# Optimization experiments

Measured on AMD Instinct MI355X. Metric: run time of the kernel, lower is better.

Reference implementation:

```python
import jax, jax.numpy as jnp
import numpy as np

VOCAB, D_MODEL, HEADS, PAD_ID = 32000, 512, 8, 0
D_K = D_MODEL // HEADS
EPS = 1e-5


def pos_encoding(T, d):
    pos = jnp.arange(T, dtype=jnp.float32)[:, None]              # [T,1]
    freqs = 1.0 / (10000.0 ** (jnp.arange(0, d, 2, dtype=jnp.float32) / d))
    ang = pos * freqs                                            # [T,d/2]
    pe = jnp.zeros((T, d), dtype=jnp.float32)
    pe = pe.at[:, 0::2].set(jnp.sin(ang)).at[:, 1::2].set(jnp.cos(ang))
    return pe


def layer_norm(x, g, b):
    mu = jnp.mean(x, axis=-1, keepdims=True)
    var = jnp.var(x, axis=-1, keepdims=True)
    return (x - mu) * jax.lax.rsqrt(var + EPS) * g + b


def setup_inputs() -> dict:
    key = jax.random.key(0)
    ks = jax.random.split(key, 12)
    B, T = 4, 2048
    s = 0.02
    inp = {
        "tokens": jax.random.randint(ks[0], (B, T), 0, VOCAB),
        "emb": jax.random.normal(ks[1], (VOCAB, D_MODEL), jnp.float32) * s,
        "wq": jax.random.normal(ks[2], (D_MODEL, D_MODEL), jnp.float32) * s,
        "bq": jnp.zeros((D_MODEL,), jnp.float32),
        "wk": jax.random.normal(ks[3], (D_MODEL, D_MODEL), jnp.float32) * s,
        "bk": jnp.zeros((D_MODEL,), jnp.float32),
        "wv": jax.random.normal(ks[4], (D_MODEL, D_MODEL), jnp.float32) * s,
        "bv": jnp.zeros((D_MODEL,), jnp.float32),
        "wo": jax.random.normal(ks[5], (D_MODEL, D_MODEL), jnp.float32) * s,
        "bo": jnp.zeros((D_MODEL,), jnp.float32),
        "w1": jax.random.normal(ks[6], (D_MODEL, 2 * D_MODEL), jnp.float32) * s,
        "b1": jnp.zeros((2 * D_MODEL,), jnp.float32),
        "w2": jax.random.normal(ks[7], (2 * D_MODEL, D_MODEL), jnp.float32) * s,
        "b2": jnp.zeros((D_MODEL,), jnp.float32),
        "ln1_g": jnp.ones((D_MODEL,), jnp.float32),
        "ln1_b": jnp.zeros((D_MODEL,), jnp.float32),
        "ln2_g": jnp.ones((D_MODEL,), jnp.float32),
        "ln2_b": jnp.zeros((D_MODEL,), jnp.float32),
    }
    return inp


def reference(tokens, emb, wq, bq, wk, bk, wv, bv, wo, bo,
              w1, b1, w2, b2, ln1_g, ln1_b, ln2_g, ln2_b):
    B, T = tokens.shape
    x = emb[tokens] * jnp.sqrt(jnp.float32(D_MODEL))             # [B,T,D]
    x = x + pos_encoding(T, D_MODEL)[None]                       # add PE
    q = (x @ wq + bq).reshape(B, T, HEADS, D_K)
    k = (x @ wk + bk).reshape(B, T, HEADS, D_K)
    v = (x @ wv + bv).reshape(B, T, HEADS, D_K)
    scores = jnp.einsum("bqhd,bkhd->bhqk", q, k) / jnp.sqrt(jnp.float32(D_K))
    key_pad_mask = tokens == PAD_ID                              # [B,T]
    neg = jnp.finfo(scores.dtype).min
    scores = jnp.where(key_pad_mask[:, None, None, :], neg, scores)
    attn = jax.nn.softmax(scores, axis=-1)                       # [B,H,T,T]
    av = jnp.einsum("bhqk,bkhd->bqhd", attn, v).reshape(B, T, D_MODEL)
    av = av @ wo + bo
    h = layer_norm(av + x, ln1_g, ln1_b)
    ff = jax.nn.relu(h @ w1 + b1) @ w2 + b2
    out = layer_norm(h + ff, ln2_g, ln2_b)
    return out, key_pad_mask
```

## Files before the change

kernel.cpp:

```cpp
#include <hip/hip_runtime.h>
#include <hip/hip_bf16.h>
#include <math.h>

#define D_MODEL 512
#define HEADS   8
#define D_K     64
#define T_SEQ   2048
#define B_SZ    4
#define NROWS   (B_SZ * T_SEQ)
#define KVB     64

#define BM 128
#define BN 128
#define BKG 64

typedef __attribute__((ext_vector_type(8))) short short8;
typedef __attribute__((ext_vector_type(4))) float f32x4;
typedef __attribute__((ext_vector_type(4))) ushort bf16x4;
typedef __attribute__((ext_vector_type(2))) unsigned int u32x2;

typedef __attribute__((address_space(1))) const unsigned int as1_uint;
typedef __attribute__((address_space(3))) unsigned int as3_uint;

__device__ __forceinline__ ushort f2bf(float f) {
    union { float f; unsigned u; } v; v.f = f;
    unsigned u = v.u;
    unsigned r = (u + 0x7FFFu + ((u >> 16) & 1u)) >> 16;
    return (ushort)r;
}
__device__ __forceinline__ float bf2f(ushort u) {
    union { unsigned u; float f; } v; v.u = ((unsigned)u) << 16;
    return v.f;
}
__device__ __forceinline__ unsigned pk_bf16(float lo, float hi) {
    unsigned r;
    asm("v_cvt_pk_bf16_f32 %0, %1, %2" : "=v"(r) : "v"(lo), "v"(hi));
    return r;
}

__global__ __launch_bounds__(256) void k_prep(
    const int* __restrict__ tokens, const float* __restrict__ emb,
    const float* __restrict__ wq, const float* __restrict__ wk,
    const float* __restrict__ wv, const float* __restrict__ wo,
    const float* __restrict__ w1, const float* __restrict__ w2,
    const float* __restrict__ bq, const float* __restrict__ bk,
    const float* __restrict__ bv,
    float* __restrict__ xf, ushort* __restrict__ xb, float* __restrict__ mask_out,
    ushort* __restrict__ wqkvT, ushort* __restrict__ woT,
    ushort* __restrict__ w1T, ushort* __restrict__ w2T,
    float* __restrict__ bqkv, float qsc)
{
    __shared__ ushort tls[32][33];
    int bid = blockIdx.x, tid = threadIdx.x;
    if (bid < 4096) {
        int row = bid * 2 + (tid >> 7);
        int t   = row & (T_SEQ - 1);
        int tok = tokens[row];
        int t2  = tid & 127;
        if (t2 == 0) mask_out[row] = (tok == 0) ? 1.0f : 0.0f;
        const float* e = emb + (size_t)tok * D_MODEL;
#pragma unroll
        for (int i = 0; i < 4; ++i) {
            int d = t2 + 128 * i;
            float freq = exp2f(-(float)(d & ~1) * 0.025952563240330564f);
            float sn, cs;
            sincosf((float)t * freq, &sn, &cs);
            float x = e[d] * 22.627416997969522f + ((d & 1) ? cs : sn);
            xf[(size_t)row * D_MODEL + d] = x;
            xb[(size_t)row * D_MODEL + d] = f2bf(x);
        }
        return;
    }
    const float* src; ushort* dst; float scale = 1.0f; int K, N, bx, by;
    if (bid < 5120) {
        int b = bid - 4096; int z = b >> 8; int rem = b & 255;
        bx = rem & 15; by = rem >> 4; K = 512; N = 512;
        src = (z == 0) ? wq : (z == 1) ? wk : (z == 2) ? wv : wo;
        dst = (z < 3) ? wqkvT + (size_t)z * 512 * 512 : woT;
        scale = (z == 0) ? qsc : 1.0f;
    } else if (bid < 5632) {
        int b = bid - 5120; bx = b & 31; by = b >> 5; K = 512; N = 1024; src = w1; dst = w1T;
    } else if (bid < 6144) {
        int b = bid - 5632; bx = b & 15; by = b >> 4; K = 1024; N = 512; src = w2; dst = w2T;
    } else {
        int i = (bid - 6144) * 256 + tid;
        if (i < 512)       bqkv[i] = bq[i] * qsc;
        else if (i < 1024) bqkv[i] = bk[i - 512];
        else if (i < 1536) bqkv[i] = bv[i - 1024];
        return;
    }
    int tx = tid & 31, ty = tid >> 5;
    int n0 = bx * 32, k0 = by * 32;
#pragma unroll
    for (int i = 0; i < 4; ++i)
        tls[ty + i * 8][tx] = f2bf(src[(size_t)(k0 + ty + i * 8) * N + n0 + tx] * scale);
    __syncthreads();
#pragma unroll
    for (int i = 0; i < 4; ++i)
        dst[(size_t)(n0 + ty + i * 8) * K + k0 + tx] = tls[tx][ty + i * 8];
}

template<int MODE, bool RELU>
__global__ __launch_bounds__(256) void k_gemm_lds(
    const ushort* __restrict__ A, const ushort* __restrict__ BT,
    const float* __restrict__ bias, void* __restrict__ C0,
    void* __restrict__ C1, void* __restrict__ C2,
    int M, int N, int K)
{
    __shared__ __attribute__((aligned(16))) ushort As[2][BM * BKG];
    __shared__ __attribute__((aligned(16))) ushort Bs[2][BN * BKG];

    const int tid = threadIdx.x;
    const int w = tid >> 6, l = tid & 63;
    const int lr = l & 15, lg = l >> 4;
    const int wr = w >> 1, wc = w & 1;

    int bx = blockIdx.x, by = blockIdx.y;
    {
        int nx = gridDim.x, ny = gridDim.y;
        if ((ny & 7) == 0) {
            int lin = bx + nx * by;
            int xcd = lin & 7, idx = lin >> 3;
            int per = ny >> 3;
            by = xcd * per + (idx % per);
            bx = idx / per;
        }
    }
    const int brow0 = by * BM;
    const int bcol0 = bx * BN;
    const int gi0 = w * 256 + l;
    const int swz = lr & 7;

    f32x4 acc[4][4] = {};
    const int nks = K >> 6;

#define STAGE(buf, k0)                                                          \
    {                                                                           \
        _Pragma("unroll")                                                       \
        for (int i = 0; i < 4; ++i) {                                           \
            int gi = gi0 + i * 64;                                              \
            int row = gi >> 3, slot = gi & 7;                                   \
            int g = slot ^ (row & 7);                                           \
            __builtin_amdgcn_global_load_lds(                                   \
                (as1_uint*)(A + (size_t)(brow0 + row) * K + (k0) + g * 8),      \
                (as3_uint*)(&As[buf][gi * 8]), 16, 0, 0);                       \
            __builtin_amdgcn_global_load_lds(                                   \
                (as1_uint*)(BT + (size_t)(bcol0 + row) * K + (k0) + g * 8),     \
                (as3_uint*)(&Bs[buf][gi * 8]), 16, 0, 0);                       \
        }                                                                       \
    }

    STAGE(0, 0);
    __syncthreads();

    int buf = 0;
    for (int ks = 0; ks < nks; ++ks) {
        if (ks + 1 < nks) STAGE(buf ^ 1, (ks + 1) * BKG);
#pragma unroll
        for (int kk = 0; kk < 2; ++kk) {
            short8 af[4], bfr[4];
#pragma unroll
            for (int m = 0; m < 4; ++m) {
                int row = wr * 64 + m * 16 + lr;
                int slot = (kk * 4 + lg) ^ swz;
                af[m] = *(const short8*)(&As[buf][row * 64 + slot * 8]);
            }
#pragma unroll
            for (int n = 0; n < 4; ++n) {
                int row = wc * 64 + n * 16 + lr;
                int slot = (kk * 4 + lg) ^ swz;
                bfr[n] = *(const short8*)(&Bs[buf][row * 64 + slot * 8]);
            }
#pragma unroll
            for (int m = 0; m < 4; ++m)
#pragma unroll
                for (int n = 0; n < 4; ++n)
                    acc[m][n] = __builtin_amdgcn_mfma_f32_16x16x32_bf16(af[m], bfr[n], acc[m][n], 0, 0, 0);
        }
        __syncthreads();
        buf ^= 1;
    }
#undef STAGE

#pragma unroll
    for (int n = 0; n < 4; ++n) {
        int col = bcol0 + wc * 64 + n * 16 + lr;
        float bv = bias[col];
#pragma unroll
        for (int m = 0; m < 4; ++m) {
            int row0 = brow0 + wr * 64 + m * 16 + 4 * lg;
            if constexpr (MODE == 2) {
                int seg = col >> 9, lc = col & 511;
                if (seg == 2) {
                    bf16x4 pk;
#pragma unroll
                    for (int j = 0; j < 4; ++j) pk[j] = f2bf(acc[m][n][j] + bv);
                    *(bf16x4*)((ushort*)C2 + (size_t)lc * M + row0) = pk;
                } else {
                    ushort* dst = (seg == 0) ? (ushort*)C0 : (ushort*)C1;
#pragma unroll
                    for (int j = 0; j < 4; ++j)
                        dst[(size_t)(row0 + j) * 512 + lc] = f2bf(acc[m][n][j] + bv);
                }
            } else if constexpr (MODE == 0) {
#pragma unroll
                for (int j = 0; j < 4; ++j) {
                    float v = acc[m][n][j] + bv;
                    if (RELU) v = fmaxf(v, 0.0f);
                    ((ushort*)C0)[(size_t)(row0 + j) * N + col] = f2bf(v);
                }
            } else {
#pragma unroll
                for (int j = 0; j < 4; ++j)
                    ((float*)C0)[(size_t)(row0 + j) * N + col] = acc[m][n][j] + bv;
            }
        }
    }
}

__global__ __launch_bounds__(512, 4) void k_attn(
    const ushort* __restrict__ Q, const ushort* __restrict__ Kb,
    const ushort* __restrict__ Vt, const int* __restrict__ tokens,
    ushort* __restrict__ Out)
{
    __shared__ __attribute__((aligned(16))) ushort Kl[2][KVB * 64];
    __shared__ __attribute__((aligned(16))) ushort Vl[2][KVB * 64];
    __shared__ ushort Pl[8][16 * 64];
    __shared__ float  Mb[T_SEQ];
    __shared__ int    padf[T_SEQ / KVB];

    const int tid = threadIdx.x;
    const int w = tid >> 6, l = tid & 63;
    const int lr = l & 15, lg = l >> 4;
    const int swz  = lr & 7;
    const int swzP = (lr ^ (lr >> 3)) & 7;

    int lin = blockIdx.x + 16 * (blockIdx.y + 8 * blockIdx.z);
    int xcd = lin & 7, idx = lin >> 3;
    int qt = idx & 15;
    int hb = xcd * 4 + (idx >> 4);
    int h = hb & 7, b = hb >> 3;

    const int q0 = qt * 128 + w * 16;

    const int gi   = w * 64 + l;
    const int srow = gi >> 3;
    const int sg   = (gi & 7) ^ (srow & 7);
    const ushort* Ksrc = Kb + ((size_t)(b * T_SEQ) + srow) * D_MODEL + h * D_K + sg * 8;
    const ushort* Vsrc = Vt + (size_t)(h * D_K + srow) * NROWS + b * T_SEQ + sg * 8;

#define ASTAGE(bufi, kt_)                                                       \
    {                                                                           \
        __builtin_amdgcn_global_load_lds(                                       \
            (as1_uint*)(Ksrc + (size_t)(kt_) * KVB * D_MODEL),                  \
            (as3_uint*)(&Kl[bufi][gi * 8]), 16, 0, 0);                          \
        __builtin_amdgcn_global_load_lds(                                       \
            (as1_uint*)(Vsrc + (kt_) * KVB),                                    \
            (as3_uint*)(&Vl[bufi][gi * 8]), 16, 0, 0);                          \
    }

    const ushort* Qh = Q + (size_t)b * T_SEQ * D_MODEL + h * D_K;
    short8 aq[2];
#pragma unroll
    for (int c2 = 0; c2 < 2; ++c2)
        aq[c2] = *(const short8*)(Qh + (size_t)(q0 + lr) * D_MODEL + c2 * 32 + 8 * lg);

    const int* tk = tokens + b * T_SEQ;
#pragma unroll
    for (int it = 0; it < T_SEQ / 512; ++it) {
        int i = tid + it * 512;
        bool pad = (tk[i] == 0);
        Mb[i] = pad ? -1e30f : 0.0f;
        unsigned long long bal = __ballot(pad);
        if (l == 0) padf[it * 8 + w] = (bal != 0ull);
    }

    float l_run = 0.0f;
    f32x4 acc[4] = {};

    ASTAGE(0, 0);
    __syncthreads();

    int buf = 0;
    const int NT = T_SEQ / KVB;
    for (int kt = 0; kt < NT; ++kt) {
        if (kt + 1 < NT) ASTAGE(buf ^ 1, kt + 1);

        const ushort* Kt = Kl[buf];
        const ushort* Vb = Vl[buf];
        ushort* P = Pl[w];

        f32x4 s[4];
        __builtin_amdgcn_s_setprio(1);
#pragma unroll
        for (int kb = 0; kb < 4; ++kb) {
            f32x4 sf = {};
#pragma unroll
            for (int c2 = 0; c2 < 2; ++c2) {
                short8 bk = *(const short8*)((const char*)Kt
                            + (kb * 16 + lr) * 128 + (((c2 * 4 + lg) ^ swz) * 16));
                sf = __builtin_amdgcn_mfma_f32_16x16x32_bf16(bk, aq[c2], sf, 0, 0, 0);
            }
            s[kb] = sf;
        }
        __builtin_amdgcn_s_setprio(0);

        if (padf[kt]) {
            const float* mrow = Mb + kt * KVB + 4 * lg;
#pragma unroll
            for (int kb = 0; kb < 4; ++kb) {
                f32x4 mb4 = *(const f32x4*)(mrow + kb * 16);
#pragma unroll
                for (int j = 0; j < 4; ++j) s[kb][j] += mb4[j];
            }
        }

        float pv[4][4];
        float ts = 0.0f;
#pragma unroll
        for (int kb = 0; kb < 4; ++kb)
#pragma unroll
            for (int j = 0; j < 4; ++j) {
                float pe = exp2f(s[kb][j]);
                pv[kb][j] = pe;
                ts += pe;
            }
        ts += __shfl_xor(ts, 16);
        ts += __shfl_xor(ts, 32);
        l_run += ts;

#pragma unroll
        for (int kb = 0; kb < 4; ++kb) {
            u32x2 dw;
            dw[0] = pk_bf16(pv[kb][0], pv[kb][1]);
            dw[1] = pk_bf16(pv[kb][2], pv[kb][3]);
            int g = (2 * kb + (lg >> 1)) ^ swzP;
            *(u32x2*)((char*)P + lr * 128 + g * 16 + (lg & 1) * 8) = dw;
        }

        short8 pa[2];
#pragma unroll
        for (int kk = 0; kk < 2; ++kk)
            pa[kk] = *(const short8*)((const char*)P + lr * 128 + (((kk * 4 + lg) ^ swzP) * 16));

        __builtin_amdgcn_s_setprio(1);
#pragma unroll
        for (int c = 0; c < 4; ++c)
#pragma unroll
            for (int kk = 0; kk < 2; ++kk) {
                short8 bv = *(const short8*)((const char*)Vb
                            + (c * 16 + lr) * 128 + (((kk * 4 + lg) ^ swz) * 16));
                acc[c] = __builtin_amdgcn_mfma_f32_16x16x32_bf16(bv, pa[kk], acc[c], 0, 0, 0);
            }
        __builtin_amdgcn_s_setprio(0);

        __syncthreads();
        buf ^= 1;
    }
#undef ASTAGE

    float rl = 1.0f / l_run;
    ushort* orow = Out + (size_t)(b * T_SEQ + q0 + lr) * D_MODEL + h * D_K;
#pragma unroll
    for (int c = 0; c < 4; ++c) {
        bf16x4 pk;
#pragma unroll
        for (int j = 0; j < 4; ++j) pk[j] = f2bf(acc[c][j] * rl);
        *(bf16x4*)(orow + c * 16 + 4 * lg) = pk;
    }
}

template<bool A_BF16, bool RES_BF16, bool OUT_F32>
__global__ __launch_bounds__(256) void k_ln(
    const void* __restrict__ A, const void* __restrict__ Res,
    const float* __restrict__ g, const float* __restrict__ bb,
    float* __restrict__ of, ushort* __restrict__ ob)
{
    int row = blockIdx.x * 4 + (threadIdx.x >> 6);
    int l = threadIdx.x & 63;
    float v[8];
    float s = 0.0f, ss = 0.0f;
#pragma unroll
    for (int i = 0; i < 2; ++i) {
        int d0 = i * 256 + l * 4;
        f32x4 va, vb;
        if (A_BF16) {
            bf16x4 t = *(const bf16x4*)((const ushort*)A + (size_t)row * D_MODEL + d0);
#pragma unroll
            for (int j = 0; j < 4; ++j) va[j] = bf2f(t[j]);
        } else {
            va = *(const f32x4*)((const float*)A + (size_t)row * D_MODEL + d0);
        }
        if (RES_BF16) {
            bf16x4 t = *(const bf16x4*)((const ushort*)Res + (size_t)row * D_MODEL + d0);
#pragma unroll
            for (int j = 0; j < 4; ++j) vb[j] = bf2f(t[j]);
        } else {
            vb = *(const f32x4*)((const float*)Res + (size_t)row * D_MODEL + d0);
        }
#pragma unroll
        for (int j = 0; j < 4; ++j) {
            float x = va[j] + vb[j];
            v[i * 4 + j] = x; s += x; ss += x * x;
        }
    }
#pragma unroll
    for (int d = 1; d < 64; d <<= 1) { s += __shfl_xor(s, d); ss += __shfl_xor(ss, d); }
    float mu  = s * (1.0f / 512.0f);
    float var = ss * (1.0f / 512.0f) - mu * mu;
    float rs  = rsqrtf(var + 1e-5f);
#pragma unroll
    for (int i = 0; i < 2; ++i)
#pragma unroll
        for (int j = 0; j < 4; ++j) {
            int d = i * 256 + l * 4 + j;
            float o = (v[i * 4 + j] - mu) * rs * g[d] + bb[d];
            if (OUT_F32) of[(size_t)row * D_MODEL + d] = o;
            else         ob[(size_t)row * D_MODEL + d] = f2bf(o);
        }
}

extern "C" void kernel_launch(void* const* d_in, const int* in_sizes, int n_in,
                              void* d_out, int out_size, void* d_ws, size_t ws_size,
                              hipStream_t stream)
{
    const int*   tokens = (const int*)  d_in[0];
    const float* emb    = (const float*)d_in[1];
    const float* wq     = (const float*)d_in[2];
    const float* bq     = (const float*)d_in[3];
    const float* wk     = (const float*)d_in[4];
    const float* bk     = (const float*)d_in[5];
    const float* wv     = (const float*)d_in[6];
    const float* bv     = (const float*)d_in[7];
    const float* wo     = (const float*)d_in[8];
    const float* bo     = (const float*)d_in[9];
    const float* w1     = (const float*)d_in[10];
    const float* b1     = (const float*)d_in[11];
    const float* w2     = (const float*)d_in[12];
    const float* b2     = (const float*)d_in[13];
    const float* ln1_g  = (const float*)d_in[14];
    const float* ln1_b  = (const float*)d_in[15];
    const float* ln2_g  = (const float*)d_in[16];
    const float* ln2_b  = (const float*)d_in[17];

    char* ws = (char*)d_ws;
    float*  xf   = (float*)(ws + 0);
    ushort* xb   = (ushort*)(ws + 16777216);
    ushort* Qb   = (ushort*)(ws + 25165824);
    ushort* Kbuf = (ushort*)(ws + 33554432);
    ushort* Vt   = (ushort*)(ws + 41943040);
    ushort* AVb  = (ushort*)(ws + 50331648);
    ushort* wqkvT = (ushort*)(ws + 67108864);
    ushort* woT  = wqkvT + 1536 * 512;
    ushort* w1T  = woT + 262144;
    ushort* w2T  = w1T + 524288;
    float*  bqkv = (float*)(w2T + 524288);

    ushort* atb  = xb;
    ushort* hb   = Qb;
    ushort* ff1b = Kbuf;
    ushort* ff2b = AVb;

    float* out_f    = (float*)d_out;
    float* mask_out = out_f + (size_t)NROWS * D_MODEL;

    const float QSC = 0.18033688011112042f;

    k_prep<<<6150, 256, 0, stream>>>(
        tokens, emb, wq, wk, wv, wo, w1, w2, bq, bk, bv,
        xf, xb, mask_out, wqkvT, woT, w1T, w2T, bqkv, QSC);

    k_gemm_lds<2, false><<<dim3(12, 64), 256, 0, stream>>>(
        xb, wqkvT, bqkv, Qb, Kbuf, Vt, NROWS, 1536, 512);

    k_attn<<<dim3(T_SEQ / 128, HEADS, B_SZ), 512, 0, stream>>>(Qb, Kbuf, Vt, tokens, atb);

    k_gemm_lds<0, false><<<dim3(4, 64), 256, 0, stream>>>(
        atb, woT, bo, AVb, nullptr, nullptr, NROWS, 512, 512);

    k_ln<true, false, false><<<NROWS / 4, 256, 0, stream>>>(
        AVb, xf, ln1_g, ln1_b, nullptr, hb);

    k_gemm_lds<0, true><<<dim3(8, 64), 256, 0, stream>>>(
        hb, w1T, b1, ff1b, nullptr, nullptr, NROWS, 1024, 512);
    k_gemm_lds<0, false><<<dim3(4, 64), 256, 0, stream>>>(
        ff1b, w2T, b2, ff2b, nullptr, nullptr, NROWS, 512, 1024);

    k_ln<true, true, true><<<NROWS / 4, 256, 0, stream>>>(
        ff2b, hb, ln2_g, ln2_b, out_f, nullptr);
}
```

Baseline: 162.3 us.

## Keep attention P in registers via permuted V layout; drop fp32 residual copy

The attention kernel now stages V through registers with a k-permuted LDS layout, so the bf16 probabilities can feed the PV MFMA straight from registers. This removes the per-wave P scratch round trip through LDS and shrinks shared memory (bf16 pad mask, no P buffer), with the occupancy hint raised from 4 to 6. Separately, the fp32 copy of the embedded input is no longer written; LayerNorm 1 reads the bf16 residual instead. That saves 16 MB of write and read traffic but lowers residual precision, and V loads now go through VGPRs rather than direct global-to-LDS.

```diff
diff --git a/kernel.cpp b/kernel.cpp
--- a/kernel.cpp
+++ b/kernel.cpp
@@ -17,7 +17,7 @@
 typedef __attribute__((ext_vector_type(8))) short short8;
 typedef __attribute__((ext_vector_type(4))) float f32x4;
 typedef __attribute__((ext_vector_type(4))) ushort bf16x4;
-typedef __attribute__((ext_vector_type(2))) unsigned int u32x2;
+typedef __attribute__((ext_vector_type(4))) unsigned int u32x4;
 
 typedef __attribute__((address_space(1))) const unsigned int as1_uint;
 typedef __attribute__((address_space(3))) unsigned int as3_uint;
@@ -45,7 +45,7 @@
     const float* __restrict__ w1, const float* __restrict__ w2,
     const float* __restrict__ bq, const float* __restrict__ bk,
     const float* __restrict__ bv,
-    float* __restrict__ xf, ushort* __restrict__ xb, float* __restrict__ mask_out,
+    ushort* __restrict__ xb, float* __restrict__ mask_out,
     ushort* __restrict__ wqkvT, ushort* __restrict__ woT,
     ushort* __restrict__ w1T, ushort* __restrict__ w2T,
     float* __restrict__ bqkv, float qsc)
@@ -66,7 +66,6 @@
             float sn, cs;
             sincosf((float)t * freq, &sn, &cs);
             float x = e[d] * 22.627416997969522f + ((d & 1) ? cs : sn);
-            xf[(size_t)row * D_MODEL + d] = x;
             xb[(size_t)row * D_MODEL + d] = f2bf(x);
         }
         return;
@@ -218,22 +217,20 @@
     }
 }
 
-__global__ __launch_bounds__(512, 4) void k_attn(
+__global__ __launch_bounds__(512, 6) void k_attn(
     const ushort* __restrict__ Q, const ushort* __restrict__ Kb,
     const ushort* __restrict__ Vt, const int* __restrict__ tokens,
     ushort* __restrict__ Out)
 {
     __shared__ __attribute__((aligned(16))) ushort Kl[2][KVB * 64];
     __shared__ __attribute__((aligned(16))) ushort Vl[2][KVB * 64];
-    __shared__ ushort Pl[8][16 * 64];
-    __shared__ float  Mb[T_SEQ];
-    __shared__ int    padf[T_SEQ / KVB];
+    __shared__ __attribute__((aligned(16))) ushort Mbh[T_SEQ];
+    __shared__ int padf[T_SEQ / KVB];
 
     const int tid = threadIdx.x;
     const int w = tid >> 6, l = tid & 63;
     const int lr = l & 15, lg = l >> 4;
-    const int swz  = lr & 7;
-    const int swzP = (lr ^ (lr >> 3)) & 7;
+    const int swz = lr & 7;
 
     int lin = blockIdx.x + 16 * (blockIdx.y + 8 * blockIdx.z);
     int xcd = lin & 7, idx = lin >> 3;
@@ -245,19 +242,17 @@
 
     const int gi   = w * 64 + l;
     const int srow = gi >> 3;
-    const int sg   = (gi & 7) ^ (srow & 7);
-    const ushort* Ksrc = Kb + ((size_t)(b * T_SEQ) + srow) * D_MODEL + h * D_K + sg * 8;
-    const ushort* Vsrc = Vt + (size_t)(h * D_K + srow) * NROWS + b * T_SEQ + sg * 8;
-
-#define ASTAGE(bufi, kt_)                                                       \
-    {                                                                           \
-        __builtin_amdgcn_global_load_lds(                                       \
-            (as1_uint*)(Ksrc + (size_t)(kt_) * KVB * D_MODEL),                  \
-            (as3_uint*)(&Kl[bufi][gi * 8]), 16, 0, 0);                          \
-        __builtin_amdgcn_global_load_lds(                                       \
-            (as1_uint*)(Vsrc + (kt_) * KVB),                                    \
-            (as3_uint*)(&Vl[bufi][gi * 8]), 16, 0, 0);                          \
-    }
+    const int sg   = gi & 7;
+    const int sgx  = sg ^ (srow & 7);
+    const ushort* Ksrc = Kb + ((size_t)(b * T_SEQ) + srow) * D_MODEL + h * D_K + sgx * 8;
+    const int kbase = 32 * (sg >> 2) + 8 * ((sg >> 1) & 1) + 4 * (sg & 1);
+    const ushort* Vsrc = Vt + (size_t)(h * D_K + srow) * NROWS + b * T_SEQ + kbase;
+    const int vds = srow * 128 + sgx * 16;
+
+#define KSTAGE(bufi, kt_)                                                       \
+    __builtin_amdgcn_global_load_lds(                                           \
+        (as1_uint*)(Ksrc + (size_t)(kt_) * KVB * D_MODEL),                      \
+        (as3_uint*)(&Kl[bufi][gi * 8]), 16, 0, 0);
 
     const ushort* Qh = Q + (size_t)b * T_SEQ * D_MODEL + h * D_K;
     short8 aq[2];
@@ -270,7 +265,7 @@
     for (int it = 0; it < T_SEQ / 512; ++it) {
         int i = tid + it * 512;
         bool pad = (tk[i] == 0);
-        Mb[i] = pad ? -1e30f : 0.0f;
+        Mbh[i] = pad ? (ushort)0xFF7F : (ushort)0;
         unsigned long long bal = __ballot(pad);
         if (l == 0) padf[it * 8 + w] = (bal != 0ull);
     }
@@ -278,17 +273,29 @@
     float l_run = 0.0f;
     f32x4 acc[4] = {};
 
-    ASTAGE(0, 0);
+    {
+        bf16x4 va = *(const bf16x4*)(Vsrc);
+        bf16x4 vb2 = *(const bf16x4*)(Vsrc + 16);
+        KSTAGE(0, 0);
+        u32x4 pk = { ((const unsigned*)&va)[0], ((const unsigned*)&va)[1],
+                     ((const unsigned*)&vb2)[0], ((const unsigned*)&vb2)[1] };
+        *(u32x4*)((char*)Vl[0] + vds) = pk;
+    }
     __syncthreads();
 
     int buf = 0;
     const int NT = T_SEQ / KVB;
     for (int kt = 0; kt < NT; ++kt) {
-        if (kt + 1 < NT) ASTAGE(buf ^ 1, kt + 1);
+        bf16x4 vna, vnb;
+        bool more = (kt + 1 < NT);
+        if (more) {
+            KSTAGE(buf ^ 1, kt + 1);
+            vna = *(const bf16x4*)(Vsrc + (kt + 1) * KVB);
+            vnb = *(const bf16x4*)(Vsrc + (kt + 1) * KVB + 16);
+        }
 
         const ushort* Kt = Kl[buf];
         const ushort* Vb = Vl[buf];
-        ushort* P = Pl[w];
 
         f32x4 s[4];
         __builtin_amdgcn_s_setprio(1);
@@ -306,12 +313,12 @@
         __builtin_amdgcn_s_setprio(0);
 
         if (padf[kt]) {
-            const float* mrow = Mb + kt * KVB + 4 * lg;
+            const ushort* mrow = Mbh + kt * KVB + 4 * lg;
 #pragma unroll
             for (int kb = 0; kb < 4; ++kb) {
-                f32x4 mb4 = *(const f32x4*)(mrow + kb * 16);
-#pragma unroll
-                for (int j = 0; j < 4; ++j) s[kb][j] += mb4[j];
+                bf16x4 m4 = *(const bf16x4*)(mrow + kb * 16);
+#pragma unroll
+                for (int j = 0; j < 4; ++j) s[kb][j] += bf2f(m4[j]);
             }
         }
 
@@ -329,35 +336,38 @@
         ts += __shfl_xor(ts, 32);
         l_run += ts;
 
+        unsigned dw[4][2];
 #pragma unroll
         for (int kb = 0; kb < 4; ++kb) {
-            u32x2 dw;
-            dw[0] = pk_bf16(pv[kb][0], pv[kb][1]);
-            dw[1] = pk_bf16(pv[kb][2], pv[kb][3]);
-            int g = (2 * kb + (lg >> 1)) ^ swzP;
-            *(u32x2*)((char*)P + lr * 128 + g * 16 + (lg & 1) * 8) = dw;
-        }
-
-        short8 pa[2];
-#pragma unroll
-        for (int kk = 0; kk < 2; ++kk)
-            pa[kk] = *(const short8*)((const char*)P + lr * 128 + (((kk * 4 + lg) ^ swzP) * 16));
+            dw[kb][0] = pk_bf16(pv[kb][0], pv[kb][1]);
+            dw[kb][1] = pk_bf16(pv[kb][2], pv[kb][3]);
+        }
+        u32x4 pw0 = { dw[0][0], dw[0][1], dw[1][0], dw[1][1] };
+        u32x4 pw1 = { dw[2][0], dw[2][1], dw[3][0], dw[3][1] };
+        short8 pa0 = __builtin_bit_cast(short8, pw0);
+        short8 pa1 = __builtin_bit_cast(short8, pw1);
 
         __builtin_amdgcn_s_setprio(1);
 #pragma unroll
-        for (int c = 0; c < 4; ++c)
-#pragma unroll
-            for (int kk = 0; kk < 2; ++kk) {
-                short8 bv = *(const short8*)((const char*)Vb
-                            + (c * 16 + lr) * 128 + (((kk * 4 + lg) ^ swz) * 16));
-                acc[c] = __builtin_amdgcn_mfma_f32_16x16x32_bf16(bv, pa[kk], acc[c], 0, 0, 0);
-            }
+        for (int c = 0; c < 4; ++c) {
+            short8 bv0 = *(const short8*)((const char*)Vb
+                         + (c * 16 + lr) * 128 + ((lg ^ swz) * 16));
+            acc[c] = __builtin_amdgcn_mfma_f32_16x16x32_bf16(bv0, pa0, acc[c], 0, 0, 0);
+            short8 bv1 = *(const short8*)((const char*)Vb
+                         + (c * 16 + lr) * 128 + (((4 + lg) ^ swz) * 16));
+            acc[c] = __builtin_amdgcn_mfma_f32_16x16x32_bf16(bv1, pa1, acc[c], 0, 0, 0);
+        }
         __builtin_amdgcn_s_setprio(0);
 
+        if (more) {
+            u32x4 pk = { ((const unsigned*)&vna)[0], ((const unsigned*)&vna)[1],
+                         ((const unsigned*)&vnb)[0], ((const unsigned*)&vnb)[1] };
+            *(u32x4*)((char*)Vl[buf ^ 1] + vds) = pk;
+        }
         __syncthreads();
         buf ^= 1;
     }
-#undef ASTAGE
+#undef KSTAGE
 
     float rl = 1.0f / l_run;
     ushort* orow = Out + (size_t)(b * T_SEQ + q0 + lr) * D_MODEL + h * D_K;
@@ -444,19 +454,18 @@
     const float* ln2_b  = (const float*)d_in[17];
 
     char* ws = (char*)d_ws;
-    float*  xf   = (float*)(ws + 0);
-    ushort* xb   = (ushort*)(ws + 16777216);
-    ushort* Qb   = (ushort*)(ws + 25165824);
-    ushort* Kbuf = (ushort*)(ws + 33554432);
-    ushort* Vt   = (ushort*)(ws + 41943040);
-    ushort* AVb  = (ushort*)(ws + 50331648);
-    ushort* wqkvT = (ushort*)(ws + 67108864);
+    ushort* xb   = (ushort*)(ws + 0);
+    ushort* Qb   = (ushort*)(ws + 8388608);
+    ushort* Kbuf = (ushort*)(ws + 16777216);
+    ushort* Vt   = (ushort*)(ws + 25165824);
+    ushort* atb  = (ushort*)(ws + 33554432);
+    ushort* AVb  = (ushort*)(ws + 41943040);
+    ushort* wqkvT = (ushort*)(ws + 50331648);
     ushort* woT  = wqkvT + 1536 * 512;
     ushort* w1T  = woT + 262144;
     ushort* w2T  = w1T + 524288;
     float*  bqkv = (float*)(w2T + 524288);
 
-    ushort* atb  = xb;
     ushort* hb   = Qb;
     ushort* ff1b = Kbuf;
     ushort* ff2b = AVb;
@@ -468,7 +477,7 @@
 
     k_prep<<<6150, 256, 0, stream>>>(
         tokens, emb, wq, wk, wv, wo, w1, w2, bq, bk, bv,
-        xf, xb, mask_out, wqkvT, woT, w1T, w2T, bqkv, QSC);
+        xb, mask_out, wqkvT, woT, w1T, w2T, bqkv, QSC);
 
     k_gemm_lds<2, false><<<dim3(12, 64), 256, 0, stream>>>(
         xb, wqkvT, bqkv, Qb, Kbuf, Vt, NROWS, 1536, 512);
@@ -478,8 +487,8 @@
     k_gemm_lds<0, false><<<dim3(4, 64), 256, 0, stream>>>(
         atb, woT, bo, AVb, nullptr, nullptr, NROWS, 512, 512);
 
-    k_ln<true, false, false><<<NROWS / 4, 256, 0, stream>>>(
-        AVb, xf, ln1_g, ln1_b, nullptr, hb);
+    k_ln<true, true, false><<<NROWS / 4, 256, 0, stream>>>(
+        AVb, xb, ln1_g, ln1_b, nullptr, hb);
 
     k_gemm_lds<0, true><<<dim3(8, 64), 256, 0, stream>>>(
         hb, w1T, b1, ff1b, nullptr, nullptr, NROWS, 1024, 512);
```

Result: no change. 159.4 us (-1.7%).
